# Kernel optimization log

Measured on AMD Instinct MI355X. Metric: run time of the kernel, lower is better.

Reference implementation:

```python
import jax, jax.numpy as jnp
import numpy as np

FRAME_SIZE = 160
AVG_POOL_K = 4
ENV_DIM = FRAME_SIZE // AVG_POOL_K + 1  # 41
FEATURE_DIM = 128
LOG_EPS = 0.5 ** 16


def causal_conv_k2(x, W, b):
    """Conv1d(kernel=2) with left pad 1 (causal), channels-last.
    x: (B, T, Cin), W: (Cout, Cin, 2) torch layout, b: (Cout,) -> (B, T, Cout)."""
    prev = jnp.pad(x, ((0, 0), (1, 0), (0, 0)))[:, :-1]  # x shifted right by 1
    return (jnp.einsum('btc,oc->bto', prev, W[:, :, 0])
            + jnp.einsum('btc,oc->bto', x, W[:, :, 1]) + b)


def setup_inputs() -> dict:
    key = jax.random.key(0)
    ks = jax.random.split(key, 6)
    B, T = 64, 2000
    N = T * FRAME_SIZE
    s = 0.05  # small init so exp() stays well-behaved
    return {
        "x": jax.random.normal(ks[0], (B, 1, N), jnp.float32),
        "features": jax.random.normal(ks[1], (B, T, FEATURE_DIM), jnp.float32),
        "W1f": (jax.random.normal(ks[2], (FRAME_SIZE, FEATURE_DIM, 2), jnp.float32) * s),
        "b1f": jnp.zeros((FRAME_SIZE,), jnp.float32),
        "W1t": (jax.random.normal(ks[3], (FRAME_SIZE, ENV_DIM, 2), jnp.float32) * s),
        "b1t": jnp.zeros((FRAME_SIZE,), jnp.float32),
        "W2": (jax.random.normal(ks[4], (FRAME_SIZE, FRAME_SIZE, 2), jnp.float32) * s),
        "b2": jnp.zeros((FRAME_SIZE,), jnp.float32),
    }


def reference(x, features, W1f, b1f, W1t, b1t, W2, b2):
    B, _, N = x.shape
    T = features.shape[1]
    # --- envelope_transform (pool_after=False) ---
    xa = jnp.abs(x[:, 0, :]).reshape(B, N // AVG_POOL_K, AVG_POOL_K).mean(-1)
    e = jnp.log(xa + LOG_EPS).reshape(B, T, ENV_DIM - 1)  # (B, T, 40)
    avg = e.mean(-1, keepdims=True)
    tenv = jnp.concatenate([e - avg, avg], axis=-1)  # (B, T, ENV_DIM)
    # --- shaping gain alpha ---
    alpha = causal_conv_k2(features, W1f, b1f) + causal_conv_k2(tenv, W1t, b1t)
    alpha = jax.nn.leaky_relu(alpha, 0.2)
    alpha = jnp.exp(causal_conv_k2(alpha, W2, b2))  # (B, T, frame_size)
    y = alpha * x.reshape(B, T, FRAME_SIZE)
    return y.reshape(B, 1, N)
```

## Files before the change

kernel.cpp:

```cpp
#include <hip/hip_runtime.h>

typedef __attribute__((ext_vector_type(8))) short short8;
typedef __attribute__((ext_vector_type(4))) float f32x4;

#define BB 64
#define TS 2000
#define NN (TS*160)
#define MB 63
#define TB 32
#define NTH 640
#define EPS_LOG 1.52587890625e-05f

#define W1F_U 0
#define W1T_U 40960
#define W2_U  61440
#define B1C_F 56320
#define B2C_F 56480

__device__ __forceinline__ unsigned short f2bf(float f) {
    union { float f; unsigned u; } v; v.f = f;
    unsigned r = v.u + 0x7FFF + ((v.u >> 16) & 1);
    return (unsigned short)(r >> 16);
}

__global__ void repack(const float* __restrict__ W1f, const float* __restrict__ b1f,
                       const float* __restrict__ W1t, const float* __restrict__ b1t,
                       const float* __restrict__ W2,  const float* __restrict__ b2,
                       void* wsv) {
    unsigned short* wu = (unsigned short*)wsv;
    float* wf = (float*)wsv;
    int n = blockIdx.x * 256 + threadIdx.x;
    if (n < 40960) {
        int tap = n / 20480, m = n % 20480;
        int ct = m / 2048, m2 = m % 2048;
        int kp = m2 / 128, col = (m2 % 128) / 8, i = m2 % 8;
        int o = ct * 16 + col, c = kp * 8 + i;
        wu[W1F_U + n] = f2bf(W1f[(o * 128 + c) * 2 + tap]);
    } else if (n < 61440) {
        int r = n - 40960;
        int tap = r / 10240, m = r % 10240;
        int ct = m / 1024, m2 = m % 1024;
        int kp = m2 / 128, col = (m2 % 128) / 8, i = m2 % 8;
        int o = ct * 16 + col, c = kp * 8 + i;
        unsigned short v = 0;
        if (c < 40) {
            float S = 0.f;
            for (int g = 0; g < 40; ++g) S += W1t[(o * 41 + g) * 2 + tap];
            float w40 = W1t[(o * 41 + 40) * 2 + tap];
            v = f2bf(W1t[(o * 41 + c) * 2 + tap] + (w40 - S) * 0.025f);
        }
        wu[W1T_U + r] = v;
    } else if (n < 112640) {
        int r = n - 61440;
        int tap = r / 25600, m = r % 25600;
        int ct = m / 2560, m2 = m % 2560;
        int kp = m2 / 128, col = (m2 % 128) / 8, i = m2 % 8;
        int o = ct * 16 + col, c = kp * 8 + i;
        wu[W2_U + r] = f2bf(W2[(o * 160 + c) * 2 + tap]);
    } else if (n < 112800) {
        int o = n - 112640;
        wf[B1C_F + o] = b1f[o] + b1t[o];
    } else if (n < 112960) {
        int o = n - 112800;
        wf[B2C_F + o] = b2[o];
    }
}

__global__ __launch_bounds__(NTH, 5) void td_main(
    const float* __restrict__ x,
    const float* __restrict__ feat,
    const unsigned short* __restrict__ wu,
    const float* __restrict__ wf,
    float* __restrict__ out)
{
    __shared__ __align__(16) unsigned short s_feat[65 * 136];
    __shared__ __align__(16) unsigned short s_e   [65 * 72];
    __shared__ __align__(16) unsigned short s_hid [64 * 168];

    const int tid  = threadIdx.x;
    const int b    = blockIdx.y;
    const int t0   = blockIdx.x * MB;
    const int wid  = tid >> 6;
    const int lane = tid & 63;
    const int lr   = lane & 15;
    const int lk   = lane >> 4;
    const int ct   = wid;
    const int cbase = lk * 8;

    const float4* feat4 = (const float4*)feat;
    const float4* x4    = (const float4*)x;

    short8 w0[6], w1[6];
    {
        const unsigned short* bf0 = wu + W1F_U + ct * 2048 + lk * 128 + lr * 8;
        const unsigned short* bt0 = wu + W1T_U + ct * 1024 + lk * 128 + lr * 8;
#pragma unroll
        for (int s = 0; s < 4; ++s) {
            w0[s] = *(const short8*)(bf0 + s * 512);
            w1[s] = *(const short8*)(bf0 + 20480 + s * 512);
        }
#pragma unroll
        for (int s = 0; s < 2; ++s) {
            w0[4 + s] = *(const short8*)(bt0 + s * 512);
            w1[4 + s] = *(const short8*)(bt0 + 10240 + s * 512);
        }
    }
    const float4 bias1 = *(const float4*)&wf[B1C_F + ct * 16 + lk * 4];

    for (int idx = tid; idx < 65 * 32; idx += NTH) {
        int r = idx >> 5, c4 = idx & 31;
        int t = t0 - 2 + r;
        float4 v = make_float4(0.f, 0.f, 0.f, 0.f);
        if (t >= 0 && t < TS) v = feat4[((size_t)b * TS + t) * 32 + c4];
        ushort4 h;
        h.x = f2bf(v.x); h.y = f2bf(v.y); h.z = f2bf(v.z); h.w = f2bf(v.w);
        *(ushort4*)&s_feat[r * 136 + c4 * 4] = h;
    }
    for (int idx = tid; idx < 65 * 40; idx += NTH) {
        int r = idx / 40, g = idx - r * 40;
        int t = t0 - 2 + r;
        unsigned short u = 0;
        if (t >= 0 && t < TS) {
            float4 v = x4[((size_t)b * NN + (size_t)t * 160 + g * 4) >> 2];
            float m = 0.25f * (fabsf(v.x) + fabsf(v.y) + fabsf(v.z) + fabsf(v.w));
            u = f2bf(__logf(m + EPS_LOG));
        }
        s_e[r * 72 + g] = u;
    }
    if (tid < 65 * 3) {
        int r = tid / 3, sgm = tid - r * 3;
        short8 z = {0, 0, 0, 0, 0, 0, 0, 0};
        *(short8*)&s_e[r * 72 + 40 + sgm * 8] = z;
    }
    __syncthreads();

#pragma unroll 2
    for (int tile = 0; tile < 4; ++tile) {
        const int rB = tile * 16 + lr;
        const unsigned short* f0 = &s_feat[rB * 136 + cbase];
        const unsigned short* e0 = &s_e[rB * 72 + cbase];
        f32x4 acc0 = {0.f, 0.f, 0.f, 0.f};
        f32x4 acc1 = {0.f, 0.f, 0.f, 0.f};
#pragma unroll
        for (int s = 0; s < 4; ++s) {
            short8 a0 = *(const short8*)(f0 + 32 * s);
            short8 a1 = *(const short8*)(f0 + 136 + 32 * s);
            acc0 = __builtin_amdgcn_mfma_f32_16x16x32_bf16(w0[s], a0, acc0, 0, 0, 0);
            acc1 = __builtin_amdgcn_mfma_f32_16x16x32_bf16(w1[s], a1, acc1, 0, 0, 0);
        }
#pragma unroll
        for (int s = 0; s < 2; ++s) {
            short8 a0 = *(const short8*)(e0 + 32 * s);
            short8 a1 = *(const short8*)(e0 + 72 + 32 * s);
            acc0 = __builtin_amdgcn_mfma_f32_16x16x32_bf16(w0[4 + s], a0, acc0, 0, 0, 0);
            acc1 = __builtin_amdgcn_mfma_f32_16x16x32_bf16(w1[4 + s], a1, acc1, 0, 0, 0);
        }
        const int th = t0 - 1 + rB;
        ushort4 pk;
        {
            float v0 = acc0[0] + acc1[0] + bias1.x; v0 = v0 >= 0.f ? v0 : 0.2f * v0;
            float v1 = acc0[1] + acc1[1] + bias1.y; v1 = v1 >= 0.f ? v1 : 0.2f * v1;
            float v2 = acc0[2] + acc1[2] + bias1.z; v2 = v2 >= 0.f ? v2 : 0.2f * v2;
            float v3 = acc0[3] + acc1[3] + bias1.w; v3 = v3 >= 0.f ? v3 : 0.2f * v3;
            pk.x = f2bf(v0); pk.y = f2bf(v1); pk.z = f2bf(v2); pk.w = f2bf(v3);
        }
        if (th < 0) pk = make_ushort4(0, 0, 0, 0);
        *(ushort4*)&s_hid[rB * 168 + ct * 16 + lk * 4] = pk;
    }

    __builtin_amdgcn_sched_barrier(0);

    {
        const unsigned short* b2p = wu + W2_U + ct * 2560 + lk * 128 + lr * 8;
#pragma unroll
        for (int s = 0; s < 5; ++s) {
            w0[s] = *(const short8*)(b2p + s * 512);
            w1[s] = *(const short8*)(b2p + 25600 + s * 512);
        }
    }
    const float4 bias2 = *(const float4*)&wf[B2C_F + ct * 16 + lk * 4];

    __syncthreads();

#pragma unroll
    for (int tile = 0; tile < 4; ++tile) {
        const int rC  = tile * 16 + lr;
        const int rCc = rC < 63 ? rC : 62;
        const unsigned short* hb = &s_hid[rCc * 168 + cbase];
        f32x4 acc0 = {0.f, 0.f, 0.f, 0.f};
        f32x4 acc1 = {0.f, 0.f, 0.f, 0.f};
#pragma unroll
        for (int s = 0; s < 5; ++s) {
            short8 a0 = *(const short8*)(hb + 32 * s);
            short8 a1 = *(const short8*)(hb + 168 + 32 * s);
            acc0 = __builtin_amdgcn_mfma_f32_16x16x32_bf16(w0[s], a0, acc0, 0, 0, 0);
            acc1 = __builtin_amdgcn_mfma_f32_16x16x32_bf16(w1[s], a1, acc1, 0, 0, 0);
        }
        const int t = t0 + rC;
        if (rC < MB && t < TS) {
            size_t off = (size_t)b * NN + (size_t)t * 160 + ct * 16 + lk * 4;
            float4 xv = *(const float4*)&x[off];
            float4 yv;
            yv.x = __expf(acc0[0] + acc1[0] + bias2.x) * xv.x;
            yv.y = __expf(acc0[1] + acc1[1] + bias2.y) * xv.y;
            yv.z = __expf(acc0[2] + acc1[2] + bias2.z) * xv.z;
            yv.w = __expf(acc0[3] + acc1[3] + bias2.w) * xv.w;
            *(float4*)&out[off] = yv;
        }
    }
}

extern "C" void kernel_launch(void* const* d_in, const int* in_sizes, int n_in,
                              void* d_out, int out_size, void* d_ws, size_t ws_size,
                              hipStream_t stream) {
    const float* x    = (const float*)d_in[0];
    const float* feat = (const float*)d_in[1];
    const float* W1f  = (const float*)d_in[2];
    const float* b1f  = (const float*)d_in[3];
    const float* W1t  = (const float*)d_in[4];
    const float* b1t  = (const float*)d_in[5];
    const float* W2   = (const float*)d_in[6];
    const float* b2   = (const float*)d_in[7];
    float* out = (float*)d_out;

    repack<<<(112960 + 255) / 256, 256, 0, stream>>>(W1f, b1f, W1t, b1t, W2, b2, d_ws);
    td_main<<<dim3(TB, BB), NTH, 0, stream>>>(
        x, feat, (const unsigned short*)d_ws, (const float*)d_ws, out);
}
```

Baseline: 85.51 us.

## Halve block threads and have each wave compute two output column tiles

```diff
diff --git a/kernel.cpp b/kernel.cpp
--- a/kernel.cpp
+++ b/kernel.cpp
@@ -8,7 +8,7 @@
 #define NN (TS*160)
 #define MB 63
 #define TB 32
-#define NTH 640
+#define NTH 320
 #define EPS_LOG 1.52587890625e-05f
 
 #define W1F_U 0
@@ -66,7 +66,7 @@
     }
 }
 
-__global__ __launch_bounds__(NTH, 5) void td_main(
+__global__ __launch_bounds__(NTH) void td_main(
     const float* __restrict__ x,
     const float* __restrict__ feat,
     const unsigned short* __restrict__ wu,
@@ -84,28 +84,32 @@
     const int lane = tid & 63;
     const int lr   = lane & 15;
     const int lk   = lane >> 4;
-    const int ct   = wid;
     const int cbase = lk * 8;
 
     const float4* feat4 = (const float4*)feat;
     const float4* x4    = (const float4*)x;
 
-    short8 w0[6], w1[6];
-    {
+    short8 wB0[2][6], wB1[2][6];
+#pragma unroll
+    for (int g = 0; g < 2; ++g) {
+        const int ct = wid * 2 + g;
         const unsigned short* bf0 = wu + W1F_U + ct * 2048 + lk * 128 + lr * 8;
         const unsigned short* bt0 = wu + W1T_U + ct * 1024 + lk * 128 + lr * 8;
 #pragma unroll
         for (int s = 0; s < 4; ++s) {
-            w0[s] = *(const short8*)(bf0 + s * 512);
-            w1[s] = *(const short8*)(bf0 + 20480 + s * 512);
+            wB0[g][s] = *(const short8*)(bf0 + s * 512);
+            wB1[g][s] = *(const short8*)(bf0 + 20480 + s * 512);
         }
 #pragma unroll
         for (int s = 0; s < 2; ++s) {
-            w0[4 + s] = *(const short8*)(bt0 + s * 512);
-            w1[4 + s] = *(const short8*)(bt0 + 10240 + s * 512);
-        }
-    }
-    const float4 bias1 = *(const float4*)&wf[B1C_F + ct * 16 + lk * 4];
+            wB0[g][4 + s] = *(const short8*)(bt0 + s * 512);
+            wB1[g][4 + s] = *(const short8*)(bt0 + 10240 + s * 512);
+        }
+    }
+    float4 bias1[2];
+#pragma unroll
+    for (int g = 0; g < 2; ++g)
+        bias1[g] = *(const float4*)&wf[B1C_F + (wid * 2 + g) * 16 + lk * 4];
 
     for (int idx = tid; idx < 65 * 32; idx += NTH) {
         int r = idx >> 5, c4 = idx & 31;
@@ -127,85 +131,103 @@
         }
         s_e[r * 72 + g] = u;
     }
-    if (tid < 65 * 3) {
-        int r = tid / 3, sgm = tid - r * 3;
+    for (int idx = tid; idx < 65 * 3; idx += NTH) {
+        int r = idx / 3, sgm = idx - r * 3;
         short8 z = {0, 0, 0, 0, 0, 0, 0, 0};
         *(short8*)&s_e[r * 72 + 40 + sgm * 8] = z;
     }
     __syncthreads();
 
-#pragma unroll 2
+#pragma unroll 1
     for (int tile = 0; tile < 4; ++tile) {
         const int rB = tile * 16 + lr;
         const unsigned short* f0 = &s_feat[rB * 136 + cbase];
         const unsigned short* e0 = &s_e[rB * 72 + cbase];
-        f32x4 acc0 = {0.f, 0.f, 0.f, 0.f};
-        f32x4 acc1 = {0.f, 0.f, 0.f, 0.f};
+        f32x4 acc0[2] = {{0.f, 0.f, 0.f, 0.f}, {0.f, 0.f, 0.f, 0.f}};
+        f32x4 acc1[2] = {{0.f, 0.f, 0.f, 0.f}, {0.f, 0.f, 0.f, 0.f}};
 #pragma unroll
         for (int s = 0; s < 4; ++s) {
             short8 a0 = *(const short8*)(f0 + 32 * s);
             short8 a1 = *(const short8*)(f0 + 136 + 32 * s);
-            acc0 = __builtin_amdgcn_mfma_f32_16x16x32_bf16(w0[s], a0, acc0, 0, 0, 0);
-            acc1 = __builtin_amdgcn_mfma_f32_16x16x32_bf16(w1[s], a1, acc1, 0, 0, 0);
+#pragma unroll
+            for (int g = 0; g < 2; ++g) {
+                acc0[g] = __builtin_amdgcn_mfma_f32_16x16x32_bf16(wB0[g][s], a0, acc0[g], 0, 0, 0);
+                acc1[g] = __builtin_amdgcn_mfma_f32_16x16x32_bf16(wB1[g][s], a1, acc1[g], 0, 0, 0);
+            }
         }
 #pragma unroll
         for (int s = 0; s < 2; ++s) {
             short8 a0 = *(const short8*)(e0 + 32 * s);
             short8 a1 = *(const short8*)(e0 + 72 + 32 * s);
-            acc0 = __builtin_amdgcn_mfma_f32_16x16x32_bf16(w0[4 + s], a0, acc0, 0, 0, 0);
-            acc1 = __builtin_amdgcn_mfma_f32_16x16x32_bf16(w1[4 + s], a1, acc1, 0, 0, 0);
+#pragma unroll
+            for (int g = 0; g < 2; ++g) {
+                acc0[g] = __builtin_amdgcn_mfma_f32_16x16x32_bf16(wB0[g][4 + s], a0, acc0[g], 0, 0, 0);
+                acc1[g] = __builtin_amdgcn_mfma_f32_16x16x32_bf16(wB1[g][4 + s], a1, acc1[g], 0, 0, 0);
+            }
         }
         const int th = t0 - 1 + rB;
-        ushort4 pk;
-        {
-            float v0 = acc0[0] + acc1[0] + bias1.x; v0 = v0 >= 0.f ? v0 : 0.2f * v0;
-            float v1 = acc0[1] + acc1[1] + bias1.y; v1 = v1 >= 0.f ? v1 : 0.2f * v1;
-            float v2 = acc0[2] + acc1[2] + bias1.z; v2 = v2 >= 0.f ? v2 : 0.2f * v2;
-            float v3 = acc0[3] + acc1[3] + bias1.w; v3 = v3 >= 0.f ? v3 : 0.2f * v3;
+#pragma unroll
+        for (int g = 0; g < 2; ++g) {
+            ushort4 pk;
+            float v0 = acc0[g][0] + acc1[g][0] + bias1[g].x; v0 = v0 >= 0.f ? v0 : 0.2f * v0;
+            float v1 = acc0[g][1] + acc1[g][1] + bias1[g].y; v1 = v1 >= 0.f ? v1 : 0.2f * v1;
+            float v2 = acc0[g][2] + acc1[g][2] + bias1[g].z; v2 = v2 >= 0.f ? v2 : 0.2f * v2;
+            float v3 = acc0[g][3] + acc1[g][3] + bias1[g].w; v3 = v3 >= 0.f ? v3 : 0.2f * v3;
             pk.x = f2bf(v0); pk.y = f2bf(v1); pk.z = f2bf(v2); pk.w = f2bf(v3);
-        }
-        if (th < 0) pk = make_ushort4(0, 0, 0, 0);
-        *(ushort4*)&s_hid[rB * 168 + ct * 16 + lk * 4] = pk;
+            if (th < 0) pk = make_ushort4(0, 0, 0, 0);
+            *(ushort4*)&s_hid[rB * 168 + (wid * 2 + g) * 16 + lk * 4] = pk;
+        }
     }
 
     __builtin_amdgcn_sched_barrier(0);
 
-    {
-        const unsigned short* b2p = wu + W2_U + ct * 2560 + lk * 128 + lr * 8;
+    short8 wC0[2][5], wC1[2][5];
+#pragma unroll
+    for (int g = 0; g < 2; ++g) {
+        const unsigned short* b2p = wu + W2_U + (wid * 2 + g) * 2560 + lk * 128 + lr * 8;
 #pragma unroll
         for (int s = 0; s < 5; ++s) {
-            w0[s] = *(const short8*)(b2p + s * 512);
-            w1[s] = *(const short8*)(b2p + 25600 + s * 512);
-        }
-    }
-    const float4 bias2 = *(const float4*)&wf[B2C_F + ct * 16 + lk * 4];
+            wC0[g][s] = *(const short8*)(b2p + s * 512);
+            wC1[g][s] = *(const short8*)(b2p + 25600 + s * 512);
+        }
+    }
+    float4 bias2[2];
+#pragma unroll
+    for (int g = 0; g < 2; ++g)
+        bias2[g] = *(const float4*)&wf[B2C_F + (wid * 2 + g) * 16 + lk * 4];
 
     __syncthreads();
 
-#pragma unroll
+#pragma unroll 1
     for (int tile = 0; tile < 4; ++tile) {
         const int rC  = tile * 16 + lr;
         const int rCc = rC < 63 ? rC : 62;
         const unsigned short* hb = &s_hid[rCc * 168 + cbase];
-        f32x4 acc0 = {0.f, 0.f, 0.f, 0.f};
-        f32x4 acc1 = {0.f, 0.f, 0.f, 0.f};
+        f32x4 acc0[2] = {{0.f, 0.f, 0.f, 0.f}, {0.f, 0.f, 0.f, 0.f}};
+        f32x4 acc1[2] = {{0.f, 0.f, 0.f, 0.f}, {0.f, 0.f, 0.f, 0.f}};
 #pragma unroll
         for (int s = 0; s < 5; ++s) {
             short8 a0 = *(const short8*)(hb + 32 * s);
             short8 a1 = *(const short8*)(hb + 168 + 32 * s);
-            acc0 = __builtin_amdgcn_mfma_f32_16x16x32_bf16(w0[s], a0, acc0, 0, 0, 0);
-            acc1 = __builtin_amdgcn_mfma_f32_16x16x32_bf16(w1[s], a1, acc1, 0, 0, 0);
+#pragma unroll
+            for (int g = 0; g < 2; ++g) {
+                acc0[g] = __builtin_amdgcn_mfma_f32_16x16x32_bf16(wC0[g][s], a0, acc0[g], 0, 0, 0);
+                acc1[g] = __builtin_amdgcn_mfma_f32_16x16x32_bf16(wC1[g][s], a1, acc1[g], 0, 0, 0);
+            }
         }
         const int t = t0 + rC;
         if (rC < MB && t < TS) {
-            size_t off = (size_t)b * NN + (size_t)t * 160 + ct * 16 + lk * 4;
-            float4 xv = *(const float4*)&x[off];
-            float4 yv;
-            yv.x = __expf(acc0[0] + acc1[0] + bias2.x) * xv.x;
-            yv.y = __expf(acc0[1] + acc1[1] + bias2.y) * xv.y;
-            yv.z = __expf(acc0[2] + acc1[2] + bias2.z) * xv.z;
-            yv.w = __expf(acc0[3] + acc1[3] + bias2.w) * xv.w;
-            *(float4*)&out[off] = yv;
+#pragma unroll
+            for (int g = 0; g < 2; ++g) {
+                size_t off = (size_t)b * NN + (size_t)t * 160 + (wid * 2 + g) * 16 + lk * 4;
+                float4 xv = *(const float4*)&x[off];
+                float4 yv;
+                yv.x = __expf(acc0[g][0] + acc1[g][0] + bias2[g].x) * xv.x;
+                yv.y = __expf(acc0[g][1] + acc1[g][1] + bias2[g].y) * xv.y;
+                yv.z = __expf(acc0[g][2] + acc1[g][2] + bias2[g].z) * xv.z;
+                yv.w = __expf(acc0[g][3] + acc1[g][3] + bias2[g].w) * xv.w;
+                *(float4*)&out[off] = yv;
+            }
         }
     }
 }
```

Result: slower. 106.4 us (+24.4%).

## Split fused kernel into hidden-layer and output kernels via global bf16 buffer

Applied to the files above, without the earlier changes.

```diff
diff --git a/kernel.cpp b/kernel.cpp
--- a/kernel.cpp
+++ b/kernel.cpp
@@ -16,6 +16,8 @@
 #define W2_U  61440
 #define B1C_F 56320
 #define B2C_F 56480
+#define HID_U 113664
+#define WS_NEED (227328ull + (unsigned long long)BB*2001*160*2)
 
 __device__ __forceinline__ unsigned short f2bf(float f) {
     union { float f; unsigned u; } v; v.f = f;
@@ -66,7 +68,168 @@
     }
 }
 
-__global__ __launch_bounds__(NTH, 5) void td_main(
+__global__ __launch_bounds__(NTH, 5) void td_hid(
+    const float* __restrict__ x,
+    const float* __restrict__ feat,
+    const unsigned short* __restrict__ wu,
+    const float* __restrict__ wf,
+    unsigned short* __restrict__ hid)
+{
+    __shared__ __align__(16) unsigned short s_feat[65 * 136];
+    __shared__ __align__(16) unsigned short s_e   [65 * 72];
+
+    const int tid  = threadIdx.x;
+    const int b    = blockIdx.y;
+    const int t0   = blockIdx.x * MB;
+    const int wid  = tid >> 6;
+    const int lane = tid & 63;
+    const int lr   = lane & 15;
+    const int lk   = lane >> 4;
+    const int ct   = wid;
+    const int cbase = lk * 8;
+
+    const float4* feat4 = (const float4*)feat;
+    const float4* x4    = (const float4*)x;
+
+    short8 w0[6], w1[6];
+    {
+        const unsigned short* bf0 = wu + W1F_U + ct * 2048 + lk * 128 + lr * 8;
+        const unsigned short* bt0 = wu + W1T_U + ct * 1024 + lk * 128 + lr * 8;
+#pragma unroll
+        for (int s = 0; s < 4; ++s) {
+            w0[s] = *(const short8*)(bf0 + s * 512);
+            w1[s] = *(const short8*)(bf0 + 20480 + s * 512);
+        }
+#pragma unroll
+        for (int s = 0; s < 2; ++s) {
+            w0[4 + s] = *(const short8*)(bt0 + s * 512);
+            w1[4 + s] = *(const short8*)(bt0 + 10240 + s * 512);
+        }
+    }
+    const float4 bias1 = *(const float4*)&wf[B1C_F + ct * 16 + lk * 4];
+
+    for (int idx = tid; idx < 65 * 32; idx += NTH) {
+        int r = idx >> 5, c4 = idx & 31;
+        int t = t0 - 2 + r;
+        float4 v = make_float4(0.f, 0.f, 0.f, 0.f);
+        if (t >= 0 && t < TS) v = feat4[((size_t)b * TS + t) * 32 + c4];
+        ushort4 h;
+        h.x = f2bf(v.x); h.y = f2bf(v.y); h.z = f2bf(v.z); h.w = f2bf(v.w);
+        *(ushort4*)&s_feat[r * 136 + c4 * 4] = h;
+    }
+    for (int idx = tid; idx < 65 * 40; idx += NTH) {
+        int r = idx / 40, g = idx - r * 40;
+        int t = t0 - 2 + r;
+        unsigned short u = 0;
+        if (t >= 0 && t < TS) {
+            float4 v = x4[((size_t)b * NN + (size_t)t * 160 + g * 4) >> 2];
+            float m = 0.25f * (fabsf(v.x) + fabsf(v.y) + fabsf(v.z) + fabsf(v.w));
+            u = f2bf(__logf(m + EPS_LOG));
+        }
+        s_e[r * 72 + g] = u;
+    }
+    if (tid < 65 * 3) {
+        int r = tid / 3, sgm = tid - r * 3;
+        short8 z = {0, 0, 0, 0, 0, 0, 0, 0};
+        *(short8*)&s_e[r * 72 + 40 + sgm * 8] = z;
+    }
+    __syncthreads();
+
+#pragma unroll 2
+    for (int tile = 0; tile < 4; ++tile) {
+        const int rB = tile * 16 + lr;
+        const unsigned short* f0 = &s_feat[rB * 136 + cbase];
+        const unsigned short* e0 = &s_e[rB * 72 + cbase];
+        f32x4 acc0 = {0.f, 0.f, 0.f, 0.f};
+        f32x4 acc1 = {0.f, 0.f, 0.f, 0.f};
+#pragma unroll
+        for (int s = 0; s < 4; ++s) {
+            short8 a0 = *(const short8*)(f0 + 32 * s);
+            short8 a1 = *(const short8*)(f0 + 136 + 32 * s);
+            acc0 = __builtin_amdgcn_mfma_f32_16x16x32_bf16(w0[s], a0, acc0, 0, 0, 0);
+            acc1 = __builtin_amdgcn_mfma_f32_16x16x32_bf16(w1[s], a1, acc1, 0, 0, 0);
+        }
+#pragma unroll
+        for (int s = 0; s < 2; ++s) {
+            short8 a0 = *(const short8*)(e0 + 32 * s);
+            short8 a1 = *(const short8*)(e0 + 72 + 32 * s);
+            acc0 = __builtin_amdgcn_mfma_f32_16x16x32_bf16(w0[4 + s], a0, acc0, 0, 0, 0);
+            acc1 = __builtin_amdgcn_mfma_f32_16x16x32_bf16(w1[4 + s], a1, acc1, 0, 0, 0);
+        }
+        const int th = t0 - 1 + rB;
+        ushort4 pk;
+        {
+            float v0 = acc0[0] + acc1[0] + bias1.x; v0 = v0 >= 0.f ? v0 : 0.2f * v0;
+            float v1 = acc0[1] + acc1[1] + bias1.y; v1 = v1 >= 0.f ? v1 : 0.2f * v1;
+            float v2 = acc0[2] + acc1[2] + bias1.z; v2 = v2 >= 0.f ? v2 : 0.2f * v2;
+            float v3 = acc0[3] + acc1[3] + bias1.w; v3 = v3 >= 0.f ? v3 : 0.2f * v3;
+            pk.x = f2bf(v0); pk.y = f2bf(v1); pk.z = f2bf(v2); pk.w = f2bf(v3);
+        }
+        if (th < 0) pk = make_ushort4(0, 0, 0, 0);
+        if (th < TS) {
+            size_t off = ((size_t)b * 2001 + (th + 1)) * 160 + ct * 16 + lk * 4;
+            *(ushort4*)&hid[off] = pk;
+        }
+    }
+}
+
+__global__ __launch_bounds__(NTH) void td_out(
+    const float* __restrict__ x,
+    const unsigned short* __restrict__ hid,
+    const unsigned short* __restrict__ wu,
+    const float* __restrict__ wf,
+    float* __restrict__ out)
+{
+    const int tid  = threadIdx.x;
+    const int b    = blockIdx.y;
+    const int t0   = blockIdx.x * MB;
+    const int wid  = tid >> 6;
+    const int lane = tid & 63;
+    const int lr   = lane & 15;
+    const int lk   = lane >> 4;
+    const int ct   = wid;
+    const int cbase = lk * 8;
+
+    short8 w0[5], w1[5];
+    {
+        const unsigned short* b2p = wu + W2_U + ct * 2560 + lk * 128 + lr * 8;
+#pragma unroll
+        for (int s = 0; s < 5; ++s) {
+            w0[s] = *(const short8*)(b2p + s * 512);
+            w1[s] = *(const short8*)(b2p + 25600 + s * 512);
+        }
+    }
+    const float4 bias2 = *(const float4*)&wf[B2C_F + ct * 16 + lk * 4];
+
+#pragma unroll 2
+    for (int tile = 0; tile < 4; ++tile) {
+        const int rC = tile * 16 + lr;
+        const int t  = t0 + rC;
+        const int tc = t < TS ? t : TS - 1;
+        const unsigned short* p0 = hid + ((size_t)b * 2001 + tc) * 160 + cbase;
+        f32x4 acc0 = {0.f, 0.f, 0.f, 0.f};
+        f32x4 acc1 = {0.f, 0.f, 0.f, 0.f};
+#pragma unroll
+        for (int s = 0; s < 5; ++s) {
+            short8 a0 = *(const short8*)(p0 + 32 * s);
+            short8 a1 = *(const short8*)(p0 + 160 + 32 * s);
+            acc0 = __builtin_amdgcn_mfma_f32_16x16x32_bf16(w0[s], a0, acc0, 0, 0, 0);
+            acc1 = __builtin_amdgcn_mfma_f32_16x16x32_bf16(w1[s], a1, acc1, 0, 0, 0);
+        }
+        if (rC < MB && t < TS) {
+            size_t off = (size_t)b * NN + (size_t)t * 160 + ct * 16 + lk * 4;
+            float4 xv = *(const float4*)&x[off];
+            float4 yv;
+            yv.x = __expf(acc0[0] + acc1[0] + bias2.x) * xv.x;
+            yv.y = __expf(acc0[1] + acc1[1] + bias2.y) * xv.y;
+            yv.z = __expf(acc0[2] + acc1[2] + bias2.z) * xv.z;
+            yv.w = __expf(acc0[3] + acc1[3] + bias2.w) * xv.w;
+            *(float4*)&out[off] = yv;
+        }
+    }
+}
+
+__global__ __launch_bounds__(NTH, 5) void td_mono(
     const float* __restrict__ x,
     const float* __restrict__ feat,
     const unsigned short* __restrict__ wu,
@@ -170,12 +333,13 @@
 
     __builtin_amdgcn_sched_barrier(0);
 
+    short8 wc0[5], wc1[5];
     {
         const unsigned short* b2p = wu + W2_U + ct * 2560 + lk * 128 + lr * 8;
 #pragma unroll
         for (int s = 0; s < 5; ++s) {
-            w0[s] = *(const short8*)(b2p + s * 512);
-            w1[s] = *(const short8*)(b2p + 25600 + s * 512);
+            wc0[s] = *(const short8*)(b2p + s * 512);
+            wc1[s] = *(const short8*)(b2p + 25600 + s * 512);
         }
     }
     const float4 bias2 = *(const float4*)&wf[B2C_F + ct * 16 + lk * 4];
@@ -193,8 +357,8 @@
         for (int s = 0; s < 5; ++s) {
             short8 a0 = *(const short8*)(hb + 32 * s);
             short8 a1 = *(const short8*)(hb + 168 + 32 * s);
-            acc0 = __builtin_amdgcn_mfma_f32_16x16x32_bf16(w0[s], a0, acc0, 0, 0, 0);
-            acc1 = __builtin_amdgcn_mfma_f32_16x16x32_bf16(w1[s], a1, acc1, 0, 0, 0);
+            acc0 = __builtin_amdgcn_mfma_f32_16x16x32_bf16(wc0[s], a0, acc0, 0, 0, 0);
+            acc1 = __builtin_amdgcn_mfma_f32_16x16x32_bf16(wc1[s], a1, acc1, 0, 0, 0);
         }
         const int t = t0 + rC;
         if (rC < MB && t < TS) {
@@ -222,8 +386,16 @@
     const float* W2   = (const float*)d_in[6];
     const float* b2   = (const float*)d_in[7];
     float* out = (float*)d_out;
+    unsigned short* wu = (unsigned short*)d_ws;
+    const float* wf    = (const float*)d_ws;
 
     repack<<<(112960 + 255) / 256, 256, 0, stream>>>(W1f, b1f, W1t, b1t, W2, b2, d_ws);
-    td_main<<<dim3(TB, BB), NTH, 0, stream>>>(
-        x, feat, (const unsigned short*)d_ws, (const float*)d_ws, out);
-}
+
+    if (ws_size >= WS_NEED) {
+        unsigned short* hid = wu + HID_U;
+        td_hid<<<dim3(TB, BB), NTH, 0, stream>>>(x, feat, wu, wf, hid);
+        td_out<<<dim3(TB, BB), NTH, 0, stream>>>(x, hid, wu, wf, out);
+    } else {
+        td_mono<<<dim3(TB, BB), NTH, 0, stream>>>(x, feat, wu, wf, out);
+    }
+}
```

Result: slower. 140.9 us (+64.7%).
